# Performance work log

Hardware: AMD Instinct MI355X
Metric: run time of the kernel (lower is better)

The kernel has to match this reference:

```python
import jax, jax.numpy as jnp
import numpy as np

E = 512      # embedding_size
H = 8        # heads
FF = 4 * E   # ffn hidden
EPS = 1e-5


def layer_norm(x, gamma, beta):
    mu = jnp.mean(x, axis=-1, keepdims=True)
    var = jnp.mean((x - mu) ** 2, axis=-1, keepdims=True)
    return (x - mu) * jax.lax.rsqrt(var + EPS) * gamma + beta


def setup_inputs() -> dict:
    key = jax.random.key(0)
    ks = jax.random.split(key, 12)
    N, L = 4, 2048
    s = E ** -0.5
    return {
        "x": jax.random.normal(ks[0], (N, L, E), jnp.float32),
        "wq": jax.random.normal(ks[1], (E, E), jnp.float32) * s,
        "wk": jax.random.normal(ks[2], (E, E), jnp.float32) * s,
        "wv": jax.random.normal(ks[3], (E, E), jnp.float32) * s,
        "wo": jax.random.normal(ks[4], (E, E), jnp.float32) * s,
        "bo": jnp.zeros((E,), jnp.float32),
        "g1": jnp.ones((E,), jnp.float32),
        "b1": jnp.zeros((E,), jnp.float32),
        "g2": jnp.ones((E,), jnp.float32),
        "b2": jnp.zeros((E,), jnp.float32),
        "w1": jax.random.normal(ks[5], (E, FF), jnp.float32) * s,
        "bf1": jnp.zeros((FF,), jnp.float32),
        "w2": jax.random.normal(ks[6], (FF, E), jnp.float32) * (FF ** -0.5),
        "bf2": jnp.zeros((E,), jnp.float32),
    }


def reference(x, wq, wk, wv, wo, bo, g1, b1, g2, b2, w1, bf1, w2, bf2):
    N, L, _ = x.shape
    skip = x
    h = layer_norm(x, g1, b1)
    # attention (weights stored as [in, out])
    q = (h @ wq).reshape(N, L, H, E // H)
    k = (h @ wk).reshape(N, L, H, E // H)
    v = (h @ wv).reshape(N, L, H, E // H)
    # NOTE: source scales by embedding_size**-0.5 (not head_dim)
    scores = jnp.einsum('nqhd,nkhd->nhqk', q, k) * (E ** -0.5)
    attn = jax.nn.softmax(scores, axis=-1)
    out = jnp.einsum('nhql,nlhd->nqhd', attn, v).reshape(N, L, E)
    x = out @ wo + bo + skip
    skip = x
    h = layer_norm(x, g2, b2)  # dropout is identity in eval
    h = jax.nn.silu(h @ w1 + bf1) @ w2 + bf2
    return h + skip
```

## Files before the change

kernel.cpp:

```cpp
#include <hip/hip_runtime.h>
#include <hip/hip_bf16.h>

typedef __bf16 bf16;
typedef __attribute__((ext_vector_type(2))) __bf16 bf16x2;
typedef __attribute__((ext_vector_type(4))) __bf16 bf16x4;
typedef __attribute__((ext_vector_type(8))) __bf16 bf16x8;
typedef __attribute__((ext_vector_type(4))) float f32x4;

#define MFMA16(a, b, c) __builtin_amdgcn_mfma_f32_16x16x32_bf16((a), (b), (c), 0, 0, 0)


__device__ __forceinline__ void load_lds16(const bf16* g, bf16* l) {
    __builtin_amdgcn_global_load_lds(
        (const __attribute__((address_space(1))) void*)g,
        (__attribute__((address_space(3))) void*)l, 16, 0, 0);
}

__device__ __forceinline__ float fexp2(float x) { return __builtin_amdgcn_exp2f(x); }

__global__ void cvt_all(const float* __restrict__ wq, const float* __restrict__ wk,
                        const float* __restrict__ wv, const float* __restrict__ wo,
                        const float* __restrict__ w1, const float* __restrict__ w2,
                        bf16* __restrict__ wqkv_t, bf16* __restrict__ wo_t,
                        bf16* __restrict__ w1_t, bf16* __restrict__ w2_t) {
    __shared__ float t[64][65];
    const int b = blockIdx.x;
    const float* src; bf16* dst;
    int sstride, dstride, r0, c0, dr0;
    if (b < 192) {
        int bx = b % 24, by = b / 24;
        int j0 = bx * 64;
        src = (j0 < 512) ? wq : (j0 < 1024) ? wk : wv;
        sstride = 512; r0 = by * 64; c0 = j0 & 511;
        dst = wqkv_t; dstride = 512; dr0 = j0;
    } else if (b < 256) {
        int tt = b - 192; int bx = tt % 8, by = tt / 8;
        src = wo; sstride = 512; r0 = by * 64; c0 = bx * 64;
        dst = wo_t; dstride = 512; dr0 = c0;
    } else if (b < 512) {
        int tt = b - 256; int bx = tt % 32, by = tt / 32;
        src = w1; sstride = 2048; r0 = by * 64; c0 = bx * 64;
        dst = w1_t; dstride = 512; dr0 = c0;
    } else {
        int tt = b - 512; int bx = tt % 8, by = tt / 8;
        src = w2; sstride = 512; r0 = by * 64; c0 = bx * 64;
        dst = w2_t; dstride = 2048; dr0 = c0;
    }
    #pragma unroll
    for (int p = 0; p < 16; p++) {
        int lin = threadIdx.x + p * 256;
        int rr = lin >> 6, cc = lin & 63;
        t[rr][cc] = src[(size_t)(r0 + rr) * sstride + c0 + cc];
    }
    __syncthreads();
    #pragma unroll
    for (int p = 0; p < 16; p++) {
        int lin = threadIdx.x + p * 256;
        int cc = lin >> 6, rr = lin & 63;
        dst[(size_t)(dr0 + cc) * dstride + r0 + rr] = (bf16)t[rr][cc];
    }
}

__global__ void ln_kernel(const float* __restrict__ x, const float* __restrict__ g,
                          const float* __restrict__ b, bf16* __restrict__ out) {
    int row = blockIdx.x * 4 + (threadIdx.x >> 6);
    int lane = threadIdx.x & 63;
    const float4* xr = (const float4*)(x + (size_t)row * 512);
    float4 v0 = xr[lane];
    float4 v1 = xr[lane + 64];
    float s  = v0.x + v0.y + v0.z + v0.w + v1.x + v1.y + v1.z + v1.w;
    float sq = v0.x*v0.x + v0.y*v0.y + v0.z*v0.z + v0.w*v0.w
             + v1.x*v1.x + v1.y*v1.y + v1.z*v1.z + v1.w*v1.w;
    #pragma unroll
    for (int d = 1; d < 64; d <<= 1) { s += __shfl_xor(s, d); sq += __shfl_xor(sq, d); }
    float mean = s * (1.f / 512.f);
    float var  = sq * (1.f / 512.f) - mean * mean;
    float rs   = rsqrtf(var + 1e-5f);
    const float4* gv = (const float4*)g;
    const float4* bv = (const float4*)b;
    float4 ga = gv[lane], gb = gv[lane + 64];
    float4 ba = bv[lane], bb = bv[lane + 64];
    bf16* orow = out + (size_t)row * 512;
    int c0 = lane * 4;
    orow[c0 + 0]   = (bf16)((v0.x - mean) * rs * ga.x + ba.x);
    orow[c0 + 1]   = (bf16)((v0.y - mean) * rs * ga.y + ba.y);
    orow[c0 + 2]   = (bf16)((v0.z - mean) * rs * ga.z + ba.z);
    orow[c0 + 3]   = (bf16)((v0.w - mean) * rs * ga.w + ba.w);
    orow[c0 + 256] = (bf16)((v1.x - mean) * rs * gb.x + bb.x);
    orow[c0 + 257] = (bf16)((v1.y - mean) * rs * gb.y + bb.y);
    orow[c0 + 258] = (bf16)((v1.z - mean) * rs * gb.z + bb.z);
    orow[c0 + 259] = (bf16)((v1.w - mean) * rs * gb.w + bb.w);
}

template<int KD, int ND, int EPI>
__global__ __launch_bounds__(256, 3) void gemm_k(
        const bf16* __restrict__ A, const bf16* __restrict__ Bt,
        const float* __restrict__ bias, void* __restrict__ outp) {
    __shared__ bf16 As[128 * 64];
    __shared__ bf16 Bs[128 * 64];
    const int bm = blockIdx.x, bn = blockIdx.y;
    const int tid = threadIdx.x;
    const int w = tid >> 6, lane = tid & 63;
    const int wm = (w >> 1) * 64, wn = (w & 1) * 64;
    const int lr = lane & 15, lq = lane >> 4, lr7 = lane & 7;
    const int srow = lane >> 3, gslot = lane & 7;
    f32x4 acc[4][4] = {};
    const bf16* Ab = A + (size_t)bm * 128 * KD;
    const bf16* Bb = Bt + (size_t)bn * 128 * KD;
    const int gcol = (gslot ^ srow) * 8;
    for (int k0 = 0; k0 < KD; k0 += 64) {
        __syncthreads();
        #pragma unroll
        for (int s = 0; s < 4; s++) {
            int rbase = w * 32 + s * 8;
            int row = rbase + srow;
            load_lds16(&Ab[(size_t)row * KD + k0 + gcol], &As[rbase * 64]);
            load_lds16(&Bb[(size_t)row * KD + k0 + gcol], &Bs[rbase * 64]);
        }
        __syncthreads();
        #pragma unroll
        for (int ks = 0; ks < 2; ks++) {
            bf16x8 af[4], bfr[4];
            #pragma unroll
            for (int mi = 0; mi < 4; mi++) {
                int row = wm + mi * 16 + lr;
                af[mi] = *(const bf16x8*)&As[row * 64 + (((ks * 4 + lq) ^ lr7) << 3)];
            }
            #pragma unroll
            for (int ni = 0; ni < 4; ni++) {
                int row = wn + ni * 16 + lr;
                bfr[ni] = *(const bf16x8*)&Bs[row * 64 + (((ks * 4 + lq) ^ lr7) << 3)];
            }
            #pragma unroll
            for (int mi = 0; mi < 4; mi++)
                #pragma unroll
                for (int ni = 0; ni < 4; ni++)
                    acc[mi][ni] = MFMA16(af[mi], bfr[ni], acc[mi][ni]);
        }
    }
    #pragma unroll
    for (int mi = 0; mi < 4; mi++)
        #pragma unroll
        for (int ni = 0; ni < 4; ni++)
            #pragma unroll
            for (int r = 0; r < 4; r++) {
                int row = bm * 128 + wm + mi * 16 + lq * 4 + r;
                int col = bn * 128 + wn + ni * 16 + lr;
                float v = acc[mi][ni][r];
                size_t off = (size_t)row * ND + col;
                if constexpr (EPI == 0) {
                    ((bf16*)outp)[off] = (bf16)v;
                } else {
                    v += bias[col];
                    v = v / (1.f + __expf(-v));
                    ((bf16*)outp)[off] = (bf16)v;
                }
            }
}

template<int KD>
__global__ __launch_bounds__(256, 4) void gemm64(
        const bf16* __restrict__ A, const bf16* __restrict__ Bt,
        const float* __restrict__ bias, const float* __restrict__ resid,
        float* __restrict__ outp) {
    __shared__ bf16 As[64 * 64];
    __shared__ bf16 Bs[64 * 64];
    const int bm = blockIdx.x, bn = blockIdx.y;
    const int tid = threadIdx.x;
    const int w = tid >> 6, lane = tid & 63;
    const int wm = (w >> 1) * 32, wn = (w & 1) * 32;
    const int lr = lane & 15, lq = lane >> 4, lr7 = lane & 7;
    const int srow = lane >> 3, gslot = lane & 7;
    f32x4 acc[2][2] = {};
    const bf16* Ab = A + (size_t)bm * 64 * KD;
    const bf16* Bb = Bt + (size_t)bn * 64 * KD;
    const int gcol = (gslot ^ srow) * 8;
    for (int k0 = 0; k0 < KD; k0 += 64) {
        __syncthreads();
        #pragma unroll
        for (int s = 0; s < 2; s++) {
            int rbase = w * 16 + s * 8;
            int row = rbase + srow;
            load_lds16(&Ab[(size_t)row * KD + k0 + gcol], &As[rbase * 64]);
            load_lds16(&Bb[(size_t)row * KD + k0 + gcol], &Bs[rbase * 64]);
        }
        __syncthreads();
        #pragma unroll
        for (int ks = 0; ks < 2; ks++) {
            bf16x8 af[2], bfr[2];
            #pragma unroll
            for (int mi = 0; mi < 2; mi++) {
                int row = wm + mi * 16 + lr;
                af[mi] = *(const bf16x8*)&As[row * 64 + (((ks * 4 + lq) ^ lr7) << 3)];
            }
            #pragma unroll
            for (int ni = 0; ni < 2; ni++) {
                int row = wn + ni * 16 + lr;
                bfr[ni] = *(const bf16x8*)&Bs[row * 64 + (((ks * 4 + lq) ^ lr7) << 3)];
            }
            #pragma unroll
            for (int mi = 0; mi < 2; mi++)
                #pragma unroll
                for (int ni = 0; ni < 2; ni++)
                    acc[mi][ni] = MFMA16(af[mi], bfr[ni], acc[mi][ni]);
        }
    }
    #pragma unroll
    for (int mi = 0; mi < 2; mi++)
        #pragma unroll
        for (int ni = 0; ni < 2; ni++)
            #pragma unroll
            for (int r = 0; r < 4; r++) {
                int row = bm * 64 + wm + mi * 16 + lq * 4 + r;
                int col = bn * 64 + wn + ni * 16 + lr;
                size_t off = (size_t)row * 512 + col;
                outp[off] = acc[mi][ni][r] + bias[col] + resid[off];
            }
}

__device__ __forceinline__ int vs_off(int d, int key) {
    int g = key >> 3;
    int sg = (g & 10) | ((g & 1) << 2) | ((g >> 2) & 1);
    sg ^= (d >> 3) & 7;
    return d * 128 + sg * 8 + (key & 7);
}

__global__ __launch_bounds__(512, 4) void attn_kernel(const bf16* __restrict__ qkv,
                                                      bf16* __restrict__ aout) {
    __shared__ bf16 Ks[128 * 64];
    __shared__ bf16 Vs[64 * 128];
    __shared__ bf16 Ps[8][16][136];
    const int b = blockIdx.x;
    const int nh = b & 31;
    const int qt = b >> 5;
    const int n = nh >> 3, h = nh & 7;
    const int tid = threadIdx.x, w = tid >> 6, lane = tid & 63;
    const int lr = lane & 15, lq = lane >> 4, lr7 = lane & 7;
    const int srow = lane >> 3, gslot = lane & 7;
    const int gcol = (gslot ^ srow) * 8;
    const float cf = 0.04419417382415922f * 1.4426950408889634f;

    const bf16* Qbase = qkv + (size_t)(n * 2048 + qt * 128 + w * 16) * 1536 + h * 64;
    bf16x8 qr0 = *(const bf16x8*)&Qbase[(size_t)lr * 1536 + lq * 8];
    bf16x8 qr1 = *(const bf16x8*)&Qbase[(size_t)lr * 1536 + 32 + lq * 8];
    bf16x8 qf[2];
    #pragma unroll
    for (int j = 0; j < 8; j++) {
        qf[0][j] = (bf16)((float)qr0[j] * cf);
        qf[1][j] = (bf16)((float)qr1[j] * cf);
    }

    f32x4 o_acc[4] = {};
    float psum[4] = {0.f, 0.f, 0.f, 0.f};

    for (int kt = 0; kt < 16; kt++) {
        const bf16* Kb = qkv + (size_t)(n * 2048 + kt * 128) * 1536 + 512 + h * 64;
        const bf16* Vb = Kb + 512;
        __syncthreads();
        #pragma unroll
        for (int s = 0; s < 2; s++) {
            int rbase = w * 16 + s * 8;
            int row = rbase + srow;
            load_lds16(&Kb[(size_t)row * 1536 + gcol], &Ks[rbase * 64]);
        }
        {
            int key = tid >> 2;
            int dq = (tid & 3) * 16;
            bf16x8 v0 = *(const bf16x8*)&Vb[(size_t)key * 1536 + dq];
            bf16x8 v1 = *(const bf16x8*)&Vb[(size_t)key * 1536 + dq + 8];
            #pragma unroll
            for (int j = 0; j < 8; j++) Vs[vs_off(dq + j, key)] = v0[j];
            #pragma unroll
            for (int j = 0; j < 8; j++) Vs[vs_off(dq + 8 + j, key)] = v1[j];
        }
        __syncthreads();

        f32x4 s[8] = {};
        #pragma unroll
        for (int kk = 0; kk < 2; kk++)
            #pragma unroll
            for (int nj = 0; nj < 8; nj++) {
                int row = nj * 16 + lr;
                bf16x8 kf = *(const bf16x8*)&Ks[row * 64 + (((kk * 4 + lq) ^ lr7) << 3)];
                s[nj] = MFMA16(qf[kk], kf, s[nj]);
            }

        #pragma unroll
        for (int r = 0; r < 4; r++) {
            #pragma unroll
            for (int nj = 0; nj < 8; nj++) {
                float p = fexp2(fminf(s[nj][r], 60.f));
                psum[r] += p;
                Ps[w][lq * 4 + r][nj * 16 + lr] = (bf16)p;
            }
        }

        #pragma unroll
        for (int kk = 0; kk < 4; kk++) {
            bf16x8 pf = *(const bf16x8*)&Ps[w][lr][kk * 32 + lq * 8];
            #pragma unroll
            for (int nj = 0; nj < 4; nj++) {
                bf16x8 vf = *(const bf16x8*)&Vs[vs_off(nj * 16 + lr, kk * 32 + lq * 8)];
                o_acc[nj] = MFMA16(pf, vf, o_acc[nj]);
            }
        }
    }

    #pragma unroll
    for (int r = 0; r < 4; r++) {
        float t = psum[r];
        #pragma unroll
        for (int d = 1; d < 16; d <<= 1) t += __shfl_xor(t, d);
        float inv = 1.f / t;
        int grow = n * 2048 + qt * 128 + w * 16 + lq * 4 + r;
        #pragma unroll
        for (int nj = 0; nj < 4; nj++)
            aout[(size_t)grow * 512 + h * 64 + nj * 16 + lr] = (bf16)(o_acc[nj][r] * inv);
    }
}

extern "C" void kernel_launch(void* const* d_in, const int* in_sizes, int n_in,
                              void* d_out, int out_size, void* d_ws, size_t ws_size,
                              hipStream_t stream) {
    (void)in_sizes; (void)n_in; (void)out_size; (void)ws_size;
    const float* x   = (const float*)d_in[0];
    const float* wq  = (const float*)d_in[1];
    const float* wk  = (const float*)d_in[2];
    const float* wv  = (const float*)d_in[3];
    const float* wo  = (const float*)d_in[4];
    const float* bo  = (const float*)d_in[5];
    const float* g1  = (const float*)d_in[6];
    const float* b1  = (const float*)d_in[7];
    const float* g2  = (const float*)d_in[8];
    const float* b2  = (const float*)d_in[9];
    const float* w1  = (const float*)d_in[10];
    const float* bf1 = (const float*)d_in[11];
    const float* w2  = (const float*)d_in[12];
    const float* bf2 = (const float*)d_in[13];
    float* out = (float*)d_out;

    char* p = (char*)d_ws;
    bf16*  h1     = (bf16*)p;  p += (size_t)8192 * 512 * 2;
    bf16*  qkvb   = (bf16*)p;  p += (size_t)8192 * 1536 * 2;
    bf16*  aout   = (bf16*)p;  p += (size_t)8192 * 512 * 2;
    float* x2     = (float*)p; p += (size_t)8192 * 512 * 4;
    bf16*  ff1    = (bf16*)p;  p += (size_t)8192 * 2048 * 2;
    bf16*  wqkv_t = (bf16*)p;  p += (size_t)1536 * 512 * 2;
    bf16*  wo_t   = (bf16*)p;  p += (size_t)512 * 512 * 2;
    bf16*  w1_t   = (bf16*)p;  p += (size_t)2048 * 512 * 2;
    bf16*  w2_t   = (bf16*)p;  p += (size_t)512 * 2048 * 2;

    cvt_all<<<768, 256, 0, stream>>>(wq, wk, wv, wo, w1, w2, wqkv_t, wo_t, w1_t, w2_t);

    ln_kernel<<<2048, 256, 0, stream>>>(x, g1, b1, h1);
    gemm_k<512, 1536, 0><<<dim3(64, 12), 256, 0, stream>>>(h1, wqkv_t, nullptr, qkvb);
    attn_kernel<<<512, 512, 0, stream>>>(qkvb, aout);
    gemm64<512><<<dim3(128, 8), 256, 0, stream>>>(aout, wo_t, bo, x, x2);
    ln_kernel<<<2048, 256, 0, stream>>>(x2, g2, b2, h1);
    gemm_k<512, 2048, 2><<<dim3(64, 16), 256, 0, stream>>>(h1, w1_t, bf1, ff1);
    gemm64<2048><<<dim3(128, 8), 256, 0, stream>>>(ff1, w2_t, bf2, x2, out);
}
```

Baseline: 251.2 us.

## Rewrite attention with 32x32 MFMA, register-resident P and pre-transposed V

Attention is rebuilt so each wave handles 32 queries with 32x32x16 MFMAs. K and a pre-transposed V are read straight from global memory instead of being staged through LDS, and P is passed between MFMAs via lane shuffles rather than an LDS buffer. A new vt_kernel transposes V into a scratch buffer that reuses the ff1 workspace. The output-projection and FFN-down GEMMs switch to 128x64 tiles, halving their block counts. This trades LDS traffic and block barriers for an extra kernel launch and uncached global reads of K and V, and the GEMMs run with fewer blocks.

New measurement: 310.9 us. 1.24x slower.

```diff
diff --git a/kernel.cpp b/kernel.cpp
--- a/kernel.cpp
+++ b/kernel.cpp
@@ -3,11 +3,12 @@
 
 typedef __bf16 bf16;
 typedef __attribute__((ext_vector_type(2))) __bf16 bf16x2;
-typedef __attribute__((ext_vector_type(4))) __bf16 bf16x4;
 typedef __attribute__((ext_vector_type(8))) __bf16 bf16x8;
 typedef __attribute__((ext_vector_type(4))) float f32x4;
+typedef __attribute__((ext_vector_type(16))) float f32x16;
 
 #define MFMA16(a, b, c) __builtin_amdgcn_mfma_f32_16x16x32_bf16((a), (b), (c), 0, 0, 0)
+#define MFMA32(a, b, c) __builtin_amdgcn_mfma_f32_32x32x16_bf16((a), (b), (c), 0, 0, 0)
 
 
 __device__ __forceinline__ void load_lds16(const bf16* g, bf16* l) {
@@ -159,37 +160,41 @@
 }
 
 template<int KD>
-__global__ __launch_bounds__(256, 4) void gemm64(
+__global__ __launch_bounds__(256, 4) void gemm_mn(
         const bf16* __restrict__ A, const bf16* __restrict__ Bt,
         const float* __restrict__ bias, const float* __restrict__ resid,
         float* __restrict__ outp) {
-    __shared__ bf16 As[64 * 64];
+    __shared__ bf16 As[128 * 64];
     __shared__ bf16 Bs[64 * 64];
     const int bm = blockIdx.x, bn = blockIdx.y;
     const int tid = threadIdx.x;
     const int w = tid >> 6, lane = tid & 63;
-    const int wm = (w >> 1) * 32, wn = (w & 1) * 32;
+    const int wm = (w >> 1) * 64, wn = (w & 1) * 32;
     const int lr = lane & 15, lq = lane >> 4, lr7 = lane & 7;
     const int srow = lane >> 3, gslot = lane & 7;
-    f32x4 acc[2][2] = {};
-    const bf16* Ab = A + (size_t)bm * 64 * KD;
+    f32x4 acc[4][2] = {};
+    const bf16* Ab = A + (size_t)bm * 128 * KD;
     const bf16* Bb = Bt + (size_t)bn * 64 * KD;
     const int gcol = (gslot ^ srow) * 8;
     for (int k0 = 0; k0 < KD; k0 += 64) {
         __syncthreads();
         #pragma unroll
-        for (int s = 0; s < 2; s++) {
-            int rbase = w * 16 + s * 8;
-            int row = rbase + srow;
-            load_lds16(&Ab[(size_t)row * KD + k0 + gcol], &As[rbase * 64]);
-            load_lds16(&Bb[(size_t)row * KD + k0 + gcol], &Bs[rbase * 64]);
+        for (int s = 0; s < 4; s++) {
+            int rbase = w * 32 + s * 8;
+            load_lds16(&Ab[(size_t)(rbase + srow) * KD + k0 + gcol], &As[rbase * 64]);
+        }
+        {
+            int rbase = w * 16;
+            load_lds16(&Bb[(size_t)(rbase + srow) * KD + k0 + gcol], &Bs[rbase * 64]);
+            rbase += 8;
+            load_lds16(&Bb[(size_t)(rbase + srow) * KD + k0 + gcol], &Bs[rbase * 64]);
         }
         __syncthreads();
         #pragma unroll
         for (int ks = 0; ks < 2; ks++) {
-            bf16x8 af[2], bfr[2];
-            #pragma unroll
-            for (int mi = 0; mi < 2; mi++) {
+            bf16x8 af[4], bfr[2];
+            #pragma unroll
+            for (int mi = 0; mi < 4; mi++) {
                 int row = wm + mi * 16 + lr;
                 af[mi] = *(const bf16x8*)&As[row * 64 + (((ks * 4 + lq) ^ lr7) << 3)];
             }
@@ -199,123 +204,133 @@
                 bfr[ni] = *(const bf16x8*)&Bs[row * 64 + (((ks * 4 + lq) ^ lr7) << 3)];
             }
             #pragma unroll
-            for (int mi = 0; mi < 2; mi++)
+            for (int mi = 0; mi < 4; mi++)
                 #pragma unroll
                 for (int ni = 0; ni < 2; ni++)
                     acc[mi][ni] = MFMA16(af[mi], bfr[ni], acc[mi][ni]);
         }
     }
     #pragma unroll
-    for (int mi = 0; mi < 2; mi++)
+    for (int mi = 0; mi < 4; mi++)
         #pragma unroll
         for (int ni = 0; ni < 2; ni++)
             #pragma unroll
             for (int r = 0; r < 4; r++) {
-                int row = bm * 64 + wm + mi * 16 + lq * 4 + r;
+                int row = bm * 128 + wm + mi * 16 + lq * 4 + r;
                 int col = bn * 64 + wn + ni * 16 + lr;
                 size_t off = (size_t)row * 512 + col;
                 outp[off] = acc[mi][ni][r] + bias[col] + resid[off];
             }
 }
 
-__device__ __forceinline__ int vs_off(int d, int key) {
-    int g = key >> 3;
-    int sg = (g & 10) | ((g & 1) << 2) | ((g >> 2) & 1);
-    sg ^= (d >> 3) & 7;
-    return d * 128 + sg * 8 + (key & 7);
-}
-
-__global__ __launch_bounds__(512, 4) void attn_kernel(const bf16* __restrict__ qkv,
-                                                      bf16* __restrict__ aout) {
-    __shared__ bf16 Ks[128 * 64];
-    __shared__ bf16 Vs[64 * 128];
-    __shared__ bf16 Ps[8][16][136];
+__global__ void vt_kernel(const bf16* __restrict__ qkvb, bf16* __restrict__ Vt) {
+    __shared__ bf16 t[64 * 72];
+    const int nh = blockIdx.x & 31, lt = blockIdx.x >> 5;
+    const int n = nh >> 3, h = nh & 7;
+    const int tid = threadIdx.x;
+    #pragma unroll
+    for (int p = 0; p < 2; p++) {
+        int lin = tid + p * 256;
+        int rr = lin >> 3, cc = lin & 7;
+        bf16x8 v = *(const bf16x8*)&qkvb[(size_t)(n * 2048 + lt * 64 + rr) * 1536
+                                         + 1024 + h * 64 + cc * 8];
+        *(bf16x8*)&t[rr * 72 + (cc ^ (rr & 7)) * 8] = v;
+    }
+    __syncthreads();
+    #pragma unroll
+    for (int p = 0; p < 2; p++) {
+        int lin = tid + p * 256;
+        int dd = lin & 63, llc = lin >> 6;
+        bf16x8 o;
+        #pragma unroll
+        for (int j = 0; j < 8; j++) {
+            int ll = llc * 8 + j;
+            o[j] = t[ll * 72 + (((dd >> 3) ^ (ll & 7)) * 8) + (dd & 7)];
+        }
+        *(bf16x8*)&Vt[(size_t)(nh * 64 + dd) * 2048 + lt * 64 + llc * 8] = o;
+    }
+}
+
+__global__ __launch_bounds__(256) void attn_kernel(const bf16* __restrict__ qkv,
+                                                   const bf16* __restrict__ Vt,
+                                                   bf16* __restrict__ aout) {
+    __shared__ bf16 Ot[4][32 * 72];
     const int b = blockIdx.x;
     const int nh = b & 31;
     const int qt = b >> 5;
     const int n = nh >> 3, h = nh & 7;
     const int tid = threadIdx.x, w = tid >> 6, lane = tid & 63;
-    const int lr = lane & 15, lq = lane >> 4, lr7 = lane & 7;
-    const int srow = lane >> 3, gslot = lane & 7;
-    const int gcol = (gslot ^ srow) * 8;
+    const int lq5 = lane & 31, g = lane >> 5;
     const float cf = 0.04419417382415922f * 1.4426950408889634f;
 
-    const bf16* Qbase = qkv + (size_t)(n * 2048 + qt * 128 + w * 16) * 1536 + h * 64;
-    bf16x8 qr0 = *(const bf16x8*)&Qbase[(size_t)lr * 1536 + lq * 8];
-    bf16x8 qr1 = *(const bf16x8*)&Qbase[(size_t)lr * 1536 + 32 + lq * 8];
-    bf16x8 qf[2];
-    #pragma unroll
-    for (int j = 0; j < 8; j++) {
-        qf[0][j] = (bf16)((float)qr0[j] * cf);
-        qf[1][j] = (bf16)((float)qr1[j] * cf);
-    }
-
-    f32x4 o_acc[4] = {};
-    float psum[4] = {0.f, 0.f, 0.f, 0.f};
-
-    for (int kt = 0; kt < 16; kt++) {
-        const bf16* Kb = qkv + (size_t)(n * 2048 + kt * 128) * 1536 + 512 + h * 64;
-        const bf16* Vb = Kb + 512;
-        __syncthreads();
-        #pragma unroll
-        for (int s = 0; s < 2; s++) {
-            int rbase = w * 16 + s * 8;
-            int row = rbase + srow;
-            load_lds16(&Kb[(size_t)row * 1536 + gcol], &Ks[rbase * 64]);
-        }
-        {
-            int key = tid >> 2;
-            int dq = (tid & 3) * 16;
-            bf16x8 v0 = *(const bf16x8*)&Vb[(size_t)key * 1536 + dq];
-            bf16x8 v1 = *(const bf16x8*)&Vb[(size_t)key * 1536 + dq + 8];
-            #pragma unroll
-            for (int j = 0; j < 8; j++) Vs[vs_off(dq + j, key)] = v0[j];
-            #pragma unroll
-            for (int j = 0; j < 8; j++) Vs[vs_off(dq + 8 + j, key)] = v1[j];
-        }
-        __syncthreads();
-
-        f32x4 s[8] = {};
-        #pragma unroll
-        for (int kk = 0; kk < 2; kk++)
-            #pragma unroll
-            for (int nj = 0; nj < 8; nj++) {
-                int row = nj * 16 + lr;
-                bf16x8 kf = *(const bf16x8*)&Ks[row * 64 + (((kk * 4 + lq) ^ lr7) << 3)];
-                s[nj] = MFMA16(qf[kk], kf, s[nj]);
-            }
-
-        #pragma unroll
-        for (int r = 0; r < 4; r++) {
-            #pragma unroll
-            for (int nj = 0; nj < 8; nj++) {
-                float p = fexp2(fminf(s[nj][r], 60.f));
-                psum[r] += p;
-                Ps[w][lq * 4 + r][nj * 16 + lr] = (bf16)p;
-            }
-        }
-
-        #pragma unroll
-        for (int kk = 0; kk < 4; kk++) {
-            bf16x8 pf = *(const bf16x8*)&Ps[w][lr][kk * 32 + lq * 8];
-            #pragma unroll
-            for (int nj = 0; nj < 4; nj++) {
-                bf16x8 vf = *(const bf16x8*)&Vs[vs_off(nj * 16 + lr, kk * 32 + lq * 8)];
-                o_acc[nj] = MFMA16(pf, vf, o_acc[nj]);
-            }
-        }
-    }
-
-    #pragma unroll
-    for (int r = 0; r < 4; r++) {
-        float t = psum[r];
-        #pragma unroll
-        for (int d = 1; d < 16; d <<= 1) t += __shfl_xor(t, d);
-        float inv = 1.f / t;
-        int grow = n * 2048 + qt * 128 + w * 16 + lq * 4 + r;
-        #pragma unroll
-        for (int nj = 0; nj < 4; nj++)
-            aout[(size_t)grow * 512 + h * 64 + nj * 16 + lr] = (bf16)(o_acc[nj][r] * inv);
+    const bf16* Qp = qkv + (size_t)(n * 2048 + qt * 128 + w * 32 + lq5) * 1536
+                     + h * 64 + g * 8;
+    bf16x8 qf[4];
+    #pragma unroll
+    for (int c = 0; c < 4; c++) {
+        bf16x8 raw = *(const bf16x8*)(Qp + c * 16);
+        #pragma unroll
+        for (int j = 0; j < 8; j++) qf[c][j] = (bf16)((float)raw[j] * cf);
+    }
+
+    f32x16 acc0 = {0}, acc1 = {0};
+    float psum = 0.f;
+
+    const bf16* Kbase = qkv + (size_t)(n * 2048 + lq5) * 1536 + 512 + h * 64 + g * 8;
+    const bf16* Vbase = Vt + (size_t)(nh * 64 + lq5) * 2048 + g * 8;
+
+    for (int kb = 0; kb < 64; kb++) {
+        const bf16* Kp = Kbase + (size_t)kb * 32 * 1536;
+        f32x16 st = {0};
+        #pragma unroll
+        for (int c = 0; c < 4; c++) {
+            bf16x8 kf = *(const bf16x8*)(Kp + (size_t)c * 16);
+            st = MFMA32(kf, qf[c], st);
+        }
+        uint32_t pk[8];
+        #pragma unroll
+        for (int i = 0; i < 8; i++) {
+            float p0 = fexp2(fminf(st[2 * i], 60.f));
+            float p1 = fexp2(fminf(st[2 * i + 1], 60.f));
+            psum += p0 + p1;
+            union { uint32_t u; bf16x2 h; } cvu;
+            cvu.h = bf16x2{(bf16)p0, (bf16)p1};
+            pk[i] = cvu.u;
+        }
+        #pragma unroll
+        for (int h16 = 0; h16 < 2; h16++) {
+            uint32_t s0 = g ? pk[4 * h16]     : pk[4 * h16 + 2];
+            uint32_t s1 = g ? pk[4 * h16 + 1] : pk[4 * h16 + 3];
+            uint32_t r0 = (uint32_t)__shfl_xor((int)s0, 32);
+            uint32_t r1 = (uint32_t)__shfl_xor((int)s1, 32);
+            union { uint4 u; bf16x8 v; } pf;
+            pf.u = g == 0 ? uint4{pk[4 * h16], pk[4 * h16 + 1], r0, r1}
+                          : uint4{r0, r1, pk[4 * h16 + 2], pk[4 * h16 + 3]};
+            const bf16* Vp = Vbase + kb * 32 + h16 * 16;
+            bf16x8 vf0 = *(const bf16x8*)(Vp);
+            bf16x8 vf1 = *(const bf16x8*)(Vp + (size_t)32 * 2048);
+            acc0 = MFMA32(vf0, pf.v, acc0);
+            acc1 = MFMA32(vf1, pf.v, acc1);
+        }
+    }
+
+    float tot = psum + __shfl_xor(psum, 32);
+    float inv = 1.f / tot;
+
+    bf16* ot = Ot[w];
+    #pragma unroll
+    for (int r = 0; r < 16; r++) {
+        int d0 = (r & 3) + 8 * (r >> 2) + 4 * g;
+        ot[lq5 * 72 + d0]      = (bf16)(acc0[r] * inv);
+        ot[lq5 * 72 + d0 + 32] = (bf16)(acc1[r] * inv);
+    }
+    __builtin_amdgcn_s_waitcnt(0);
+    #pragma unroll
+    for (int i = 0; i < 4; i++) {
+        int tq = i * 8 + (lane >> 3);
+        bf16x8 ov = *(const bf16x8*)&ot[tq * 72 + (lane & 7) * 8];
+        *(bf16x8*)&aout[(size_t)(n * 2048 + qt * 128 + w * 32 + tq) * 512
+                        + h * 64 + (lane & 7) * 8] = ov;
     }
 }
 
@@ -349,14 +364,16 @@
     bf16*  wo_t   = (bf16*)p;  p += (size_t)512 * 512 * 2;
     bf16*  w1_t   = (bf16*)p;  p += (size_t)2048 * 512 * 2;
     bf16*  w2_t   = (bf16*)p;  p += (size_t)512 * 2048 * 2;
+    bf16*  Vt     = (bf16*)ff1;
 
     cvt_all<<<768, 256, 0, stream>>>(wq, wk, wv, wo, w1, w2, wqkv_t, wo_t, w1_t, w2_t);
 
     ln_kernel<<<2048, 256, 0, stream>>>(x, g1, b1, h1);
     gemm_k<512, 1536, 0><<<dim3(64, 12), 256, 0, stream>>>(h1, wqkv_t, nullptr, qkvb);
-    attn_kernel<<<512, 512, 0, stream>>>(qkvb, aout);
-    gemm64<512><<<dim3(128, 8), 256, 0, stream>>>(aout, wo_t, bo, x, x2);
+    vt_kernel<<<1024, 256, 0, stream>>>(qkvb, Vt);
+    attn_kernel<<<512, 256, 0, stream>>>(qkvb, Vt, aout);
+    gemm_mn<512><<<dim3(64, 8), 256, 0, stream>>>(aout, wo_t, bo, x, x2);
     ln_kernel<<<2048, 256, 0, stream>>>(x2, g2, b2, h1);
     gemm_k<512, 2048, 2><<<dim3(64, 16), 256, 0, stream>>>(h1, w1_t, bf1, ff1);
-    gemm64<2048><<<dim3(128, 8), 256, 0, stream>>>(ff1, w2_t, bf2, x2, out);
-}
+    gemm_mn<2048><<<dim3(64, 8), 256, 0, stream>>>(ff1, w2_t, bf2, x2, out);
+}
```
